# Optimization experiments

Measured on AMD Instinct MI355X. Metric: run time of the kernel, lower is better.

## Reference

```python
import jax, jax.numpy as jnp
import numpy as np

N_NODES = 100000
N_EDGES = 1600000


def _cheb_norm(edge_index, num_nodes):
    # PyG ChebConv norm with sym normalization, lambda_max=2:
    # remove self-loops, L = I - D^-1/2 A D^-1/2, scale by 2/lambda_max (=1),
    # add self-loops with -1 -> diagonal nets to 0, leaving w = -d^-1/2 d^-1/2 on edges.
    src, dst = edge_index[0], edge_index[1]
    mask = (src != dst).astype(jnp.float32)  # remove_self_loops
    deg = jax.ops.segment_sum(mask, src, num_segments=num_nodes)
    dinv = jnp.where(deg > 0, jax.lax.rsqrt(jnp.maximum(deg, 1.0)), 0.0)
    w = -dinv[src] * dinv[dst] * mask
    return w


def _cheb_conv(x, src, dst, w_edge, W, b, num_nodes):
    # W: [K=3, C_in, C_out], Chebyshev recurrence T0=x, T1=Lx, T2=2L T1 - T0
    def prop(h):
        return jax.ops.segment_sum(w_edge[:, None] * h[src], dst, num_segments=num_nodes)

    tx0 = x
    tx1 = prop(x)
    tx2 = 2.0 * prop(tx1) - tx0
    out = tx0 @ W[0] + tx1 @ W[1] + tx2 @ W[2] + b
    return out


def setup_inputs() -> dict:
    key = jax.random.key(0)
    ks = jax.random.split(key, 10)
    x = jax.random.normal(ks[0], (N_NODES, 128), dtype=jnp.float32)
    edge_index = jax.random.randint(ks[1], (2, N_EDGES), 0, N_NODES, dtype=jnp.int64)
    batch = jnp.zeros((N_NODES,), dtype=jnp.int64)

    def glorot(k, shape):
        fan = shape[-2] + shape[-1]
        return jax.random.uniform(k, shape, jnp.float32, -1.0, 1.0) * np.sqrt(6.0 / fan)

    W1 = glorot(ks[2], (3, 128, 64))
    b1 = jnp.zeros((64,), jnp.float32)
    W2 = glorot(ks[3], (3, 64, 128))
    b2 = jnp.zeros((128,), jnp.float32)
    W3 = glorot(ks[4], (3, 128, 256))
    b3 = jnp.zeros((256,), jnp.float32)
    return {"x": x, "edge_index": edge_index, "batch": batch,
            "W1": W1, "b1": b1, "W2": W2, "b2": b2, "W3": W3, "b3": b3}


def reference(x, edge_index, batch, W1, b1, W2, b2, W3, b3):
    num_nodes = x.shape[0]
    src, dst = edge_index[0], edge_index[1]
    w_edge = _cheb_norm(edge_index, num_nodes)
    h = jax.nn.relu(_cheb_conv(x, src, dst, w_edge, W1, b1, num_nodes))
    h = jax.nn.relu(_cheb_conv(h, src, dst, w_edge, W2, b2, num_nodes))
    h = _cheb_conv(h, src, dst, w_edge, W3, b3, num_nodes)
    return h
```

## Files before the change

### kernel.cpp

```cpp
#include <hip/hip_runtime.h>

#define N_NODES 100000
#define N_EDGES 1600000
#define CAP 64

typedef short short8 __attribute__((ext_vector_type(8)));
typedef float f32x4 __attribute__((ext_vector_type(4)));

__device__ __forceinline__ unsigned short f2b(float f) {
    unsigned u = __builtin_bit_cast(unsigned, f);
    u += 0x7fffu + ((u >> 16) & 1u);
    return (unsigned short)(u >> 16);
}
__device__ __forceinline__ float b2f_lo(unsigned p) {
    return __builtin_bit_cast(float, p << 16);
}
__device__ __forceinline__ float b2f_hi(unsigned p) {
    return __builtin_bit_cast(float, p & 0xffff0000u);
}
__device__ __forceinline__ float b2f(unsigned short s) {
    return __builtin_bit_cast(float, ((unsigned)s) << 16);
}

__global__ void k_f2b(const float* __restrict__ in, unsigned short* __restrict__ out, int n4) {
    int i = blockIdx.x * blockDim.x + threadIdx.x;
    if (i < n4) {
        float4 v = ((const float4*)in)[i];
        uint2 o;
        o.x = (unsigned)f2b(v.x) | ((unsigned)f2b(v.y) << 16);
        o.y = (unsigned)f2b(v.z) | ((unsigned)f2b(v.w) << 16);
        ((uint2*)out)[i] = o;
    }
}

__global__ void k_wt(const float* __restrict__ W, unsigned short* __restrict__ Wt,
                     int KT, int COUT) {
    int i = blockIdx.x * blockDim.x + threadIdx.x;
    if (i < KT * COUT) {
        int k = i % KT, n = i / KT;
        Wt[(size_t)n * KT + k] = f2b(W[(size_t)k * COUT + n]);
    }
}

__global__ void k_build(const int* __restrict__ src, const int* __restrict__ dst,
                        float* __restrict__ degout, int* __restrict__ cnt,
                        int* __restrict__ slots) {
    int e = blockIdx.x * blockDim.x + threadIdx.x;
    if (e < N_EDGES) {
        int s = src[e], d = dst[e];
        if (s != d) {
            atomicAdd(&degout[s], 1.0f);
            int pos = atomicAdd(&cnt[d], 1);
            if (pos < CAP) slots[(size_t)d * CAP + pos] = s;
        }
    }
}

__global__ void k_dinv(float* __restrict__ deg) {
    int n = blockIdx.x * blockDim.x + threadIdx.x;
    if (n < N_NODES) {
        float dg = deg[n];
        deg[n] = dg > 0.f ? rsqrtf(dg) : 0.f;
    }
}

template <int C>
__global__ __launch_bounds__(256) void k_gather4(const unsigned short* __restrict__ h,
                                                 const int* __restrict__ cnt,
                                                 const int* __restrict__ slots,
                                                 const float* __restrict__ dinv,
                                                 float alpha, const unsigned short* __restrict__ init,
                                                 float beta, unsigned short* __restrict__ out) {
    const int wave = threadIdx.x >> 6;
    const int lane = threadIdx.x & 63;
    const int half = lane >> 5;
    const int l32  = lane & 31;
    const int n0 = (blockIdx.x * 4 + wave) * 2;
    if (n0 >= N_NODES) return;
    const int n1 = n0 + 1;
    const int m0 = min(cnt[n0], CAP);
    const int m1 = min(cnt[n1], CAP);
    const int nMy = half ? n1 : n0;
    const int mMy = half ? m1 : m0;
    (void)mMy;

    int c0l = 0, c1l = 0;
    float w0f = 0.f, w1f = 0.f;
    if (lane < m0) { c0l = slots[(size_t)n0 * CAP + lane]; w0f = dinv[c0l]; }
    if (lane < m1) { c1l = slots[(size_t)n1 * CAP + lane]; w1f = dinv[c1l]; }
    const int w0i = __builtin_bit_cast(int, w0f);
    const int w1i = __builtin_bit_cast(int, w1f);

    const int mlo = min(m0, m1), mhi = max(m0, m1);
    const float scale = -alpha * dinv[nMy];

    if (C == 128) {
        const uint2* h4 = (const uint2*)h;
        float ax = 0.f, ay = 0.f, az = 0.f, aw = 0.f;
        int j = 0;
        for (; j + 4 <= mlo; j += 4) {
            #pragma unroll
            for (int k = 0; k < 4; k++) {
                int cA = __builtin_amdgcn_readlane(c0l, j + k);
                int cB = __builtin_amdgcn_readlane(c1l, j + k);
                float wA = __builtin_bit_cast(float, __builtin_amdgcn_readlane(w0i, j + k));
                float wB = __builtin_bit_cast(float, __builtin_amdgcn_readlane(w1i, j + k));
                int c = half ? cB : cA;
                float w = half ? wB : wA;
                uint2 q = h4[(size_t)c * 32 + l32];
                ax = fmaf(w, b2f_lo(q.x), ax); ay = fmaf(w, b2f_hi(q.x), ay);
                az = fmaf(w, b2f_lo(q.y), az); aw = fmaf(w, b2f_hi(q.y), aw);
            }
        }
        for (; j < mhi; j++) {
            int cA = __builtin_amdgcn_readlane(c0l, j);
            int cB = __builtin_amdgcn_readlane(c1l, j);
            float wA = __builtin_bit_cast(float, __builtin_amdgcn_readlane(w0i, j));
            float wB = __builtin_bit_cast(float, __builtin_amdgcn_readlane(w1i, j));
            int c = half ? cB : cA;
            float w = half ? wB : wA;
            uint2 q = h4[(size_t)c * 32 + l32];
            ax = fmaf(w, b2f_lo(q.x), ax); ay = fmaf(w, b2f_hi(q.x), ay);
            az = fmaf(w, b2f_lo(q.y), az); aw = fmaf(w, b2f_hi(q.y), aw);
        }
        float vx = scale * ax, vy = scale * ay, vz = scale * az, vw = scale * aw;
        if (init) {
            uint2 ip = ((const uint2*)init)[(size_t)nMy * 32 + l32];
            vx = fmaf(beta, b2f_lo(ip.x), vx); vy = fmaf(beta, b2f_hi(ip.x), vy);
            vz = fmaf(beta, b2f_lo(ip.y), vz); vw = fmaf(beta, b2f_hi(ip.y), vw);
        }
        uint2 o;
        o.x = (unsigned)f2b(vx) | ((unsigned)f2b(vy) << 16);
        o.y = (unsigned)f2b(vz) | ((unsigned)f2b(vw) << 16);
        ((uint2*)out)[(size_t)nMy * 32 + l32] = o;
    } else {
        const unsigned* h2 = (const unsigned*)h;
        float ax = 0.f, ay = 0.f;
        int j = 0;
        for (; j + 4 <= mlo; j += 4) {
            #pragma unroll
            for (int k = 0; k < 4; k++) {
                int cA = __builtin_amdgcn_readlane(c0l, j + k);
                int cB = __builtin_amdgcn_readlane(c1l, j + k);
                float wA = __builtin_bit_cast(float, __builtin_amdgcn_readlane(w0i, j + k));
                float wB = __builtin_bit_cast(float, __builtin_amdgcn_readlane(w1i, j + k));
                int c = half ? cB : cA;
                float w = half ? wB : wA;
                unsigned q = h2[(size_t)c * 32 + l32];
                ax = fmaf(w, b2f_lo(q), ax); ay = fmaf(w, b2f_hi(q), ay);
            }
        }
        for (; j < mhi; j++) {
            int cA = __builtin_amdgcn_readlane(c0l, j);
            int cB = __builtin_amdgcn_readlane(c1l, j);
            float wA = __builtin_bit_cast(float, __builtin_amdgcn_readlane(w0i, j));
            float wB = __builtin_bit_cast(float, __builtin_amdgcn_readlane(w1i, j));
            int c = half ? cB : cA;
            float w = half ? wB : wA;
            unsigned q = h2[(size_t)c * 32 + l32];
            ax = fmaf(w, b2f_lo(q), ax); ay = fmaf(w, b2f_hi(q), ay);
        }
        float vx = scale * ax, vy = scale * ay;
        if (init) {
            unsigned ip = ((const unsigned*)init)[(size_t)nMy * 32 + l32];
            vx = fmaf(beta, b2f_lo(ip), vx); vy = fmaf(beta, b2f_hi(ip), vy);
        }
        ((unsigned*)out)[(size_t)nMy * 32 + l32] =
            (unsigned)f2b(vx) | ((unsigned)f2b(vy) << 16);
    }
}

template <int CIN, int COUT, int NSL, bool RELU, bool BF16OUT>
__global__ __launch_bounds__(256) void k_mm2(const unsigned short* __restrict__ t0,
                                             const unsigned short* __restrict__ t1,
                                             const unsigned short* __restrict__ t2,
                                             const unsigned short* __restrict__ Wt,
                                             const float* __restrict__ bias,
                                             void* __restrict__ outv) {
    constexpr int KT = 3 * CIN;
    constexpr int KP = KT + 8;
    constexpr int NFR = NSL / 16;
    __shared__ unsigned short sw[NSL * KP];

    const int tid = threadIdx.x;
    const int n0 = blockIdx.y * NSL;

    constexpr int CHUNKS = NSL * KT / 8;
    for (int i = tid; i < CHUNKS; i += 256) {
        int row = i / (KT / 8);
        int k8 = i % (KT / 8);
        short8 v = *(const short8*)(Wt + (size_t)(n0 + row) * KT + k8 * 8);
        *(short8*)(sw + row * KP + k8 * 8) = v;
    }
    __syncthreads();

    const int wave = tid >> 6, lane = tid & 63;
    const int l16 = lane & 15, quad = lane >> 4;
    const int mBase = blockIdx.x * 128 + wave * 32;
    const int r0 = mBase + l16, r1 = mBase + 16 + l16;
    const bool in0 = r0 < N_NODES, in1 = r1 < N_NODES;

    f32x4 acc[2][NFR] = {};
    const unsigned short* tb[3] = {t0, t1, t2};
    const short8 zero8 = {0, 0, 0, 0, 0, 0, 0, 0};

    #pragma unroll
    for (int kt = 0; kt < KT / 32; kt++) {
        const int kb = kt * 32;
        const unsigned short* t = tb[kb / CIN];
        const int kin = (kb % CIN) + quad * 8;
        short8 a0 = zero8, a1 = zero8;
        if (in0) a0 = *(const short8*)(t + (size_t)r0 * CIN + kin);
        if (in1) a1 = *(const short8*)(t + (size_t)r1 * CIN + kin);
        #pragma unroll
        for (int nf = 0; nf < NFR; nf++) {
            const short8 b = *(const short8*)(sw + (nf * 16 + l16) * KP + kb + quad * 8);
            acc[0][nf] = __builtin_amdgcn_mfma_f32_16x16x32_bf16(a0, b, acc[0][nf], 0, 0, 0);
            acc[1][nf] = __builtin_amdgcn_mfma_f32_16x16x32_bf16(a1, b, acc[1][nf], 0, 0, 0);
        }
    }

    #pragma unroll
    for (int mi = 0; mi < 2; mi++) {
        #pragma unroll
        for (int nf = 0; nf < NFR; nf++) {
            #pragma unroll
            for (int r = 0; r < 4; r++) {
                const int node = mBase + mi * 16 + quad * 4 + r;
                if (node < N_NODES) {
                    const int co = n0 + nf * 16 + l16;
                    float o = acc[mi][nf][r] + bias[co];
                    if (RELU) o = fmaxf(o, 0.f);
                    if (BF16OUT)
                        ((unsigned short*)outv)[(size_t)node * COUT + co] = f2b(o);
                    else
                        ((float*)outv)[(size_t)node * COUT + co] = o;
                }
            }
        }
    }
}

static inline int ceil_div(int a, int b) { return (a + b - 1) / b; }

extern "C" void kernel_launch(void* const* d_in, const int* in_sizes, int n_in,
                              void* d_out, int out_size, void* d_ws, size_t ws_size,
                              hipStream_t stream) {
    const float* x   = (const float*)d_in[0];
    const int*   ei  = (const int*)d_in[1];
    const int*   src = ei;
    const int*   dst = ei + N_EDGES;
    const float* W1 = (const float*)d_in[3];
    const float* b1 = (const float*)d_in[4];
    const float* W2 = (const float*)d_in[5];
    const float* b2 = (const float*)d_in[6];
    const float* W3 = (const float*)d_in[7];
    const float* b3 = (const float*)d_in[8];
    float* out = (float*)d_out;

    char* p = (char*)d_ws;
    int*   slots  = (int*)p;             p += (size_t)N_NODES * CAP * 4;
    float* dinv   = (float*)p;           p += (size_t)N_NODES * 4;
    int*   cnt    = (int*)p;             p += (size_t)N_NODES * 4;
    unsigned short* xb   = (unsigned short*)p; p += (size_t)N_NODES * 128 * 2;
    unsigned short* tx1b = (unsigned short*)p; p += (size_t)N_NODES * 128 * 2;
    unsigned short* tx2b = (unsigned short*)p; p += (size_t)N_NODES * 128 * 2;
    unsigned short* h1b  = (unsigned short*)p; p += (size_t)N_NODES * 64 * 2;
    unsigned short* h2b  = (unsigned short*)p; p += (size_t)N_NODES * 128 * 2;
    unsigned short* Wt1  = (unsigned short*)p; p += (size_t)64 * 384 * 2;
    unsigned short* Wt2  = (unsigned short*)p; p += (size_t)128 * 192 * 2;
    unsigned short* Wt3  = (unsigned short*)p; p += (size_t)256 * 384 * 2;

    const int TB = 256;
    const int gE = ceil_div(N_EDGES, TB);
    const int gN = ceil_div(N_NODES, TB);
    const int gG = ceil_div(N_NODES, 8);
    const int gM = ceil_div(N_NODES, 128);

    k_f2b<<<ceil_div(N_NODES * 128 / 4, TB), TB, 0, stream>>>(x, xb, N_NODES * 128 / 4);
    k_wt<<<ceil_div(384 * 64, TB), TB, 0, stream>>>(W1, Wt1, 384, 64);
    k_wt<<<ceil_div(192 * 128, TB), TB, 0, stream>>>(W2, Wt2, 192, 128);
    k_wt<<<ceil_div(384 * 256, TB), TB, 0, stream>>>(W3, Wt3, 384, 256);

    hipMemsetAsync(dinv, 0, N_NODES * sizeof(float), stream);
    hipMemsetAsync(cnt, 0, N_NODES * sizeof(int), stream);
    k_build<<<gE, TB, 0, stream>>>(src, dst, dinv, cnt, slots);
    k_dinv<<<gN, TB, 0, stream>>>(dinv);

    k_gather4<128><<<gG, TB, 0, stream>>>(xb, cnt, slots, dinv, 1.f, nullptr, 0.f, tx1b);
    k_gather4<128><<<gG, TB, 0, stream>>>(tx1b, cnt, slots, dinv, 2.f, xb, -1.f, tx2b);
    k_mm2<128, 64, 64, true, true><<<dim3(gM, 1), TB, 0, stream>>>(xb, tx1b, tx2b, Wt1, b1, h1b);

    k_gather4<64><<<gG, TB, 0, stream>>>(h1b, cnt, slots, dinv, 1.f, nullptr, 0.f, tx1b);
    k_gather4<64><<<gG, TB, 0, stream>>>(tx1b, cnt, slots, dinv, 2.f, h1b, -1.f, tx2b);
    k_mm2<64, 128, 128, true, true><<<dim3(gM, 1), TB, 0, stream>>>(h1b, tx1b, tx2b, Wt2, b2, h2b);

    k_gather4<128><<<gG, TB, 0, stream>>>(h2b, cnt, slots, dinv, 1.f, nullptr, 0.f, tx1b);
    k_gather4<128><<<gG, TB, 0, stream>>>(tx1b, cnt, slots, dinv, 2.f, h2b, -1.f, tx2b);
    k_mm2<128, 256, 64, false, false><<<dim3(gM, 4), TB, 0, stream>>>(h2b, tx1b, tx2b, Wt3, b3, out);
}
```

Before: 848.3 us.

## Project layer-1 features before propagation and keep A-fragments in registers for final matmul

Layer 1 is reformulated so the 128-wide input is first multiplied by combined Chebyshev weights down to 64-wide channels (a 192-column product: x·W1, x·W2, and x·(W0−W2)+b). The two propagations then run on 64-wide data, with the ReLU fused into the second gather, which removes the separate bf16 conversion pass over x and the layer-1 combine matmul. The final layer uses a new matmul that loads its activation fragments once and loops over all output slices in a single block, so activations are not reread once per slice. This trades extra strided reads in the gathers and a larger shared-weight reload loop for less gather traffic, with slightly different rounding order.

Result: faster. 798.7 us (-5.8%).

```diff
diff --git a/kernel.cpp b/kernel.cpp
--- a/kernel.cpp
+++ b/kernel.cpp
@@ -17,20 +17,6 @@
 }
 __device__ __forceinline__ float b2f_hi(unsigned p) {
     return __builtin_bit_cast(float, p & 0xffff0000u);
-}
-__device__ __forceinline__ float b2f(unsigned short s) {
-    return __builtin_bit_cast(float, ((unsigned)s) << 16);
-}
-
-__global__ void k_f2b(const float* __restrict__ in, unsigned short* __restrict__ out, int n4) {
-    int i = blockIdx.x * blockDim.x + threadIdx.x;
-    if (i < n4) {
-        float4 v = ((const float4*)in)[i];
-        uint2 o;
-        o.x = (unsigned)f2b(v.x) | ((unsigned)f2b(v.y) << 16);
-        o.y = (unsigned)f2b(v.z) | ((unsigned)f2b(v.w) << 16);
-        ((uint2*)out)[i] = o;
-    }
 }
 
 __global__ void k_wt(const float* __restrict__ W, unsigned short* __restrict__ Wt,
@@ -40,6 +26,23 @@
         int k = i % KT, n = i / KT;
         Wt[(size_t)n * KT + k] = f2b(W[(size_t)k * COUT + n]);
     }
+}
+
+__global__ void k_wt1m(const float* __restrict__ W, unsigned short* __restrict__ Wt) {
+    int i = blockIdx.x * blockDim.x + threadIdx.x;
+    if (i < 192 * 128) {
+        int k = i % 128, n = i / 128;
+        float v;
+        if (n < 64)       v = W[(128 + k) * 64 + n];
+        else if (n < 128) v = W[(256 + k) * 64 + (n - 64)];
+        else              v = W[(0 + k) * 64 + (n - 128)] - W[(256 + k) * 64 + (n - 128)];
+        Wt[(size_t)n * 128 + k] = f2b(v);
+    }
+}
+
+__global__ void k_bias192(const float* __restrict__ b1, float* __restrict__ bias) {
+    int i = threadIdx.x;
+    if (i < 192) bias[i] = (i >= 128) ? b1[i - 128] : 0.f;
 }
 
 __global__ void k_build(const int* __restrict__ src, const int* __restrict__ dst,
@@ -64,13 +67,17 @@
     }
 }
 
-template <int C>
-__global__ __launch_bounds__(256) void k_gather4(const unsigned short* __restrict__ h,
+template <int C, bool RELU>
+__global__ __launch_bounds__(256) void k_gather5(const unsigned short* __restrict__ h,
+                                                 int hStride,
                                                  const int* __restrict__ cnt,
                                                  const int* __restrict__ slots,
                                                  const float* __restrict__ dinv,
-                                                 float alpha, const unsigned short* __restrict__ init,
-                                                 float beta, unsigned short* __restrict__ out) {
+                                                 float alpha,
+                                                 const unsigned short* __restrict__ init,
+                                                 int iStride,
+                                                 float beta,
+                                                 unsigned short* __restrict__ out) {
     const int wave = threadIdx.x >> 6;
     const int lane = threadIdx.x & 63;
     const int half = lane >> 5;
@@ -81,8 +88,6 @@
     const int m0 = min(cnt[n0], CAP);
     const int m1 = min(cnt[n1], CAP);
     const int nMy = half ? n1 : n0;
-    const int mMy = half ? m1 : m0;
-    (void)mMy;
 
     int c0l = 0, c1l = 0;
     float w0f = 0.f, w1f = 0.f;
@@ -107,7 +112,7 @@
                 float wB = __builtin_bit_cast(float, __builtin_amdgcn_readlane(w1i, j + k));
                 int c = half ? cB : cA;
                 float w = half ? wB : wA;
-                uint2 q = h4[(size_t)c * 32 + l32];
+                uint2 q = h4[(size_t)c * hStride + l32];
                 ax = fmaf(w, b2f_lo(q.x), ax); ay = fmaf(w, b2f_hi(q.x), ay);
                 az = fmaf(w, b2f_lo(q.y), az); aw = fmaf(w, b2f_hi(q.y), aw);
             }
@@ -119,15 +124,19 @@
             float wB = __builtin_bit_cast(float, __builtin_amdgcn_readlane(w1i, j));
             int c = half ? cB : cA;
             float w = half ? wB : wA;
-            uint2 q = h4[(size_t)c * 32 + l32];
+            uint2 q = h4[(size_t)c * hStride + l32];
             ax = fmaf(w, b2f_lo(q.x), ax); ay = fmaf(w, b2f_hi(q.x), ay);
             az = fmaf(w, b2f_lo(q.y), az); aw = fmaf(w, b2f_hi(q.y), aw);
         }
         float vx = scale * ax, vy = scale * ay, vz = scale * az, vw = scale * aw;
         if (init) {
-            uint2 ip = ((const uint2*)init)[(size_t)nMy * 32 + l32];
+            uint2 ip = ((const uint2*)init)[(size_t)nMy * iStride + l32];
             vx = fmaf(beta, b2f_lo(ip.x), vx); vy = fmaf(beta, b2f_hi(ip.x), vy);
             vz = fmaf(beta, b2f_lo(ip.y), vz); vw = fmaf(beta, b2f_hi(ip.y), vw);
+        }
+        if (RELU) {
+            vx = fmaxf(vx, 0.f); vy = fmaxf(vy, 0.f);
+            vz = fmaxf(vz, 0.f); vw = fmaxf(vw, 0.f);
         }
         uint2 o;
         o.x = (unsigned)f2b(vx) | ((unsigned)f2b(vy) << 16);
@@ -146,7 +155,7 @@
                 float wB = __builtin_bit_cast(float, __builtin_amdgcn_readlane(w1i, j + k));
                 int c = half ? cB : cA;
                 float w = half ? wB : wA;
-                unsigned q = h2[(size_t)c * 32 + l32];
+                unsigned q = h2[(size_t)c * hStride + l32];
                 ax = fmaf(w, b2f_lo(q), ax); ay = fmaf(w, b2f_hi(q), ay);
             }
         }
@@ -157,14 +166,15 @@
             float wB = __builtin_bit_cast(float, __builtin_amdgcn_readlane(w1i, j));
             int c = half ? cB : cA;
             float w = half ? wB : wA;
-            unsigned q = h2[(size_t)c * 32 + l32];
+            unsigned q = h2[(size_t)c * hStride + l32];
             ax = fmaf(w, b2f_lo(q), ax); ay = fmaf(w, b2f_hi(q), ay);
         }
         float vx = scale * ax, vy = scale * ay;
         if (init) {
-            unsigned ip = ((const unsigned*)init)[(size_t)nMy * 32 + l32];
+            unsigned ip = ((const unsigned*)init)[(size_t)nMy * iStride + l32];
             vx = fmaf(beta, b2f_lo(ip), vx); vy = fmaf(beta, b2f_hi(ip), vy);
         }
+        if (RELU) { vx = fmaxf(vx, 0.f); vy = fmaxf(vy, 0.f); }
         ((unsigned*)out)[(size_t)nMy * 32 + l32] =
             (unsigned)f2b(vx) | ((unsigned)f2b(vy) << 16);
     }
@@ -235,6 +245,156 @@
                         ((unsigned short*)outv)[(size_t)node * COUT + co] = f2b(o);
                     else
                         ((float*)outv)[(size_t)node * COUT + co] = o;
+                }
+            }
+        }
+    }
+}
+
+template <int CIN, int COUT, int NSL>
+__global__ __launch_bounds__(256) void k_mm1(const float* __restrict__ x,
+                                             const unsigned short* __restrict__ Wt,
+                                             const float* __restrict__ bias,
+                                             unsigned short* __restrict__ outb) {
+    constexpr int KT = CIN;
+    constexpr int KP = KT + 8;
+    constexpr int NFR = NSL / 16;
+    __shared__ unsigned short sw[NSL * KP];
+
+    const int tid = threadIdx.x;
+    const int n0 = blockIdx.y * NSL;
+
+    constexpr int CHUNKS = NSL * KT / 8;
+    for (int i = tid; i < CHUNKS; i += 256) {
+        int row = i / (KT / 8);
+        int k8 = i % (KT / 8);
+        *(short8*)(sw + row * KP + k8 * 8) =
+            *(const short8*)(Wt + (size_t)(n0 + row) * KT + k8 * 8);
+    }
+    __syncthreads();
+
+    const int wave = tid >> 6, lane = tid & 63;
+    const int l16 = lane & 15, quad = lane >> 4;
+    const int mBase = blockIdx.x * 128 + wave * 32;
+    const int r0 = mBase + l16, r1 = mBase + 16 + l16;
+    const bool in0 = r0 < N_NODES, in1 = r1 < N_NODES;
+
+    f32x4 acc[2][NFR] = {};
+    const short8 zero8 = {0, 0, 0, 0, 0, 0, 0, 0};
+
+    #pragma unroll
+    for (int kt = 0; kt < KT / 32; kt++) {
+        const int kin = kt * 32 + quad * 8;
+        short8 a0 = zero8, a1 = zero8;
+        if (in0) {
+            const float* px = x + (size_t)r0 * CIN + kin;
+            float4 f0 = *(const float4*)px, f1 = *(const float4*)(px + 4);
+            a0[0] = (short)f2b(f0.x); a0[1] = (short)f2b(f0.y);
+            a0[2] = (short)f2b(f0.z); a0[3] = (short)f2b(f0.w);
+            a0[4] = (short)f2b(f1.x); a0[5] = (short)f2b(f1.y);
+            a0[6] = (short)f2b(f1.z); a0[7] = (short)f2b(f1.w);
+        }
+        if (in1) {
+            const float* px = x + (size_t)r1 * CIN + kin;
+            float4 f0 = *(const float4*)px, f1 = *(const float4*)(px + 4);
+            a1[0] = (short)f2b(f0.x); a1[1] = (short)f2b(f0.y);
+            a1[2] = (short)f2b(f0.z); a1[3] = (short)f2b(f0.w);
+            a1[4] = (short)f2b(f1.x); a1[5] = (short)f2b(f1.y);
+            a1[6] = (short)f2b(f1.z); a1[7] = (short)f2b(f1.w);
+        }
+        #pragma unroll
+        for (int nf = 0; nf < NFR; nf++) {
+            const short8 b = *(const short8*)(sw + (nf * 16 + l16) * KP + kt * 32 + quad * 8);
+            acc[0][nf] = __builtin_amdgcn_mfma_f32_16x16x32_bf16(a0, b, acc[0][nf], 0, 0, 0);
+            acc[1][nf] = __builtin_amdgcn_mfma_f32_16x16x32_bf16(a1, b, acc[1][nf], 0, 0, 0);
+        }
+    }
+
+    #pragma unroll
+    for (int mi = 0; mi < 2; mi++) {
+        #pragma unroll
+        for (int nf = 0; nf < NFR; nf++) {
+            #pragma unroll
+            for (int r = 0; r < 4; r++) {
+                const int node = mBase + mi * 16 + quad * 4 + r;
+                if (node < N_NODES) {
+                    const int co = n0 + nf * 16 + l16;
+                    float o = acc[mi][nf][r] + bias[co];
+                    outb[(size_t)node * COUT + co] = f2b(o);
+                }
+            }
+        }
+    }
+}
+
+template <int CIN, int COUT, int NSL>
+__global__ __launch_bounds__(256) void k_mm3(const unsigned short* __restrict__ t0,
+                                             const unsigned short* __restrict__ t1,
+                                             const unsigned short* __restrict__ t2,
+                                             const unsigned short* __restrict__ Wt,
+                                             const float* __restrict__ bias,
+                                             float* __restrict__ out) {
+    constexpr int KT = 3 * CIN;
+    constexpr int KP = KT + 8;
+    constexpr int NFR = NSL / 16;
+    constexpr int NSLICES = COUT / NSL;
+    constexpr int KSTEPS = KT / 32;
+    __shared__ unsigned short sw[NSL * KP];
+
+    const int tid = threadIdx.x;
+    const int wave = tid >> 6, lane = tid & 63;
+    const int l16 = lane & 15, quad = lane >> 4;
+    const int mBase = blockIdx.x * 128 + wave * 32;
+    const int r0 = mBase + l16, r1 = mBase + 16 + l16;
+    const bool in0 = r0 < N_NODES, in1 = r1 < N_NODES;
+
+    const unsigned short* tb[3] = {t0, t1, t2};
+    const short8 zero8 = {0, 0, 0, 0, 0, 0, 0, 0};
+
+    short8 a0[KSTEPS], a1[KSTEPS];
+    #pragma unroll
+    for (int kt = 0; kt < KSTEPS; kt++) {
+        const int kb = kt * 32;
+        const unsigned short* t = tb[kb / CIN];
+        const int kin = (kb % CIN) + quad * 8;
+        a0[kt] = in0 ? *(const short8*)(t + (size_t)r0 * CIN + kin) : zero8;
+        a1[kt] = in1 ? *(const short8*)(t + (size_t)r1 * CIN + kin) : zero8;
+    }
+
+    constexpr int CHUNKS = NSL * KT / 8;
+    for (int ns = 0; ns < NSLICES; ns++) {
+        const int n0 = ns * NSL;
+        if (ns) __syncthreads();
+        for (int i = tid; i < CHUNKS; i += 256) {
+            int row = i / (KT / 8);
+            int k8 = i % (KT / 8);
+            *(short8*)(sw + row * KP + k8 * 8) =
+                *(const short8*)(Wt + (size_t)(n0 + row) * KT + k8 * 8);
+        }
+        __syncthreads();
+
+        f32x4 acc[2][NFR] = {};
+        #pragma unroll
+        for (int kt = 0; kt < KSTEPS; kt++) {
+            #pragma unroll
+            for (int nf = 0; nf < NFR; nf++) {
+                const short8 b = *(const short8*)(sw + (nf * 16 + l16) * KP + kt * 32 + quad * 8);
+                acc[0][nf] = __builtin_amdgcn_mfma_f32_16x16x32_bf16(a0[kt], b, acc[0][nf], 0, 0, 0);
+                acc[1][nf] = __builtin_amdgcn_mfma_f32_16x16x32_bf16(a1[kt], b, acc[1][nf], 0, 0, 0);
+            }
+        }
+
+        #pragma unroll
+        for (int mi = 0; mi < 2; mi++) {
+            #pragma unroll
+            for (int nf = 0; nf < NFR; nf++) {
+                #pragma unroll
+                for (int r = 0; r < 4; r++) {
+                    const int node = mBase + mi * 16 + quad * 4 + r;
+                    if (node < N_NODES) {
+                        const int co = n0 + nf * 16 + l16;
+                        out[(size_t)node * COUT + co] = acc[mi][nf][r] + bias[co];
+                    }
                 }
             }
         }
@@ -262,14 +422,15 @@
     int*   slots  = (int*)p;             p += (size_t)N_NODES * CAP * 4;
     float* dinv   = (float*)p;           p += (size_t)N_NODES * 4;
     int*   cnt    = (int*)p;             p += (size_t)N_NODES * 4;
-    unsigned short* xb   = (unsigned short*)p; p += (size_t)N_NODES * 128 * 2;
     unsigned short* tx1b = (unsigned short*)p; p += (size_t)N_NODES * 128 * 2;
+    unsigned short* h1b  = (unsigned short*)p; p += (size_t)N_NODES * 64 * 2;
     unsigned short* tx2b = (unsigned short*)p; p += (size_t)N_NODES * 128 * 2;
-    unsigned short* h1b  = (unsigned short*)p; p += (size_t)N_NODES * 64 * 2;
     unsigned short* h2b  = (unsigned short*)p; p += (size_t)N_NODES * 128 * 2;
-    unsigned short* Wt1  = (unsigned short*)p; p += (size_t)64 * 384 * 2;
+    unsigned short* Wt1m = (unsigned short*)p; p += (size_t)192 * 128 * 2;
+    float* bias192       = (float*)p;          p += (size_t)192 * 4;
     unsigned short* Wt2  = (unsigned short*)p; p += (size_t)128 * 192 * 2;
     unsigned short* Wt3  = (unsigned short*)p; p += (size_t)256 * 384 * 2;
+    unsigned short* vub = tx2b;
 
     const int TB = 256;
     const int gE = ceil_div(N_EDGES, TB);
@@ -277,8 +438,8 @@
     const int gG = ceil_div(N_NODES, 8);
     const int gM = ceil_div(N_NODES, 128);
 
-    k_f2b<<<ceil_div(N_NODES * 128 / 4, TB), TB, 0, stream>>>(x, xb, N_NODES * 128 / 4);
-    k_wt<<<ceil_div(384 * 64, TB), TB, 0, stream>>>(W1, Wt1, 384, 64);
+    k_wt1m<<<ceil_div(192 * 128, TB), TB, 0, stream>>>(W1, Wt1m);
+    k_bias192<<<1, 192, 0, stream>>>(b1, bias192);
     k_wt<<<ceil_div(192 * 128, TB), TB, 0, stream>>>(W2, Wt2, 192, 128);
     k_wt<<<ceil_div(384 * 256, TB), TB, 0, stream>>>(W3, Wt3, 384, 256);
 
@@ -287,15 +448,21 @@
     k_build<<<gE, TB, 0, stream>>>(src, dst, dinv, cnt, slots);
     k_dinv<<<gN, TB, 0, stream>>>(dinv);
 
-    k_gather4<128><<<gG, TB, 0, stream>>>(xb, cnt, slots, dinv, 1.f, nullptr, 0.f, tx1b);
-    k_gather4<128><<<gG, TB, 0, stream>>>(tx1b, cnt, slots, dinv, 2.f, xb, -1.f, tx2b);
-    k_mm2<128, 64, 64, true, true><<<dim3(gM, 1), TB, 0, stream>>>(xb, tx1b, tx2b, Wt1, b1, h1b);
-
-    k_gather4<64><<<gG, TB, 0, stream>>>(h1b, cnt, slots, dinv, 1.f, nullptr, 0.f, tx1b);
-    k_gather4<64><<<gG, TB, 0, stream>>>(tx1b, cnt, slots, dinv, 2.f, h1b, -1.f, tx2b);
+    k_mm1<128, 192, 64><<<dim3(gM, 3), TB, 0, stream>>>(x, Wt1m, bias192, vub);
+    k_gather5<64, false><<<gG, TB, 0, stream>>>(vub + 64, 96, cnt, slots, dinv,
+                                                2.f, vub, 96, 1.f, tx1b);
+    k_gather5<64, true><<<gG, TB, 0, stream>>>(tx1b, 32, cnt, slots, dinv,
+                                               1.f, vub + 128, 96, 1.f, h1b);
+
+    k_gather5<64, false><<<gG, TB, 0, stream>>>(h1b, 32, cnt, slots, dinv,
+                                                1.f, nullptr, 0, 0.f, tx1b);
+    k_gather5<64, false><<<gG, TB, 0, stream>>>(tx1b, 32, cnt, slots, dinv,
+                                                2.f, h1b, 32, -1.f, tx2b);
     k_mm2<64, 128, 128, true, true><<<dim3(gM, 1), TB, 0, stream>>>(h1b, tx1b, tx2b, Wt2, b2, h2b);
 
-    k_gather4<128><<<gG, TB, 0, stream>>>(h2b, cnt, slots, dinv, 1.f, nullptr, 0.f, tx1b);
-    k_gather4<128><<<gG, TB, 0, stream>>>(tx1b, cnt, slots, dinv, 2.f, h2b, -1.f, tx2b);
-    k_mm2<128, 256, 64, false, false><<<dim3(gM, 4), TB, 0, stream>>>(h2b, tx1b, tx2b, Wt3, b3, out);
-}
+    k_gather5<128, false><<<gG, TB, 0, stream>>>(h2b, 32, cnt, slots, dinv,
+                                                 1.f, nullptr, 0, 0.f, tx1b);
+    k_gather5<128, false><<<gG, TB, 0, stream>>>(tx1b, 32, cnt, slots, dinv,
+                                                 2.f, h2b, 32, -1.f, tx2b);
+    k_mm3<128, 256, 64><<<dim3(gM, 1), TB, 0, stream>>>(h2b, tx1b, tx2b, Wt3, b3, out);
+}
```
